# Kernel optimization log

Measured on AMD Instinct MI355X. Metric: run time of the kernel, lower is better.

## Reference

```python
import jax, jax.numpy as jnp
import numpy as np

N = 100000   # nodes
DEG = 4      # fixed out-degree (>2 so every node survives the c>2 mask)
E = N * DEG  # edges
IN = 128
H = 256


def _lin_params(key, fan_out, fan_in, bias=True):
    k1, k2 = jax.random.split(key)
    W = 0.05 * jax.random.normal(k1, (fan_out, fan_in), jnp.float32)
    if bias:
        b = 0.05 * jax.random.normal(k2, (fan_out,), jnp.float32)
        return W, b
    return W


def setup_inputs() -> dict:
    key = jax.random.key(0)
    ks = jax.random.split(key, 12)
    x = jax.random.normal(ks[0], (N, IN), jnp.float32)
    # every node has exactly DEG outgoing edges -> out-degree 4 > 2 for all nodes
    src = jnp.repeat(jnp.arange(N, dtype=jnp.int32), DEG)
    dst = jax.random.randint(ks[1], (E,), 0, N, dtype=jnp.int32)
    edge_index = jnp.stack([src, dst])  # [2, E]
    batch = jnp.zeros((N,), jnp.int32)
    Wr0, br0 = _lin_params(ks[2], H, IN)
    Ws0 = _lin_params(ks[3], H, IN, bias=False)
    Wr1, br1 = _lin_params(ks[4], H, H)
    Ws1 = _lin_params(ks[5], H, H, bias=False)
    Wr2, br2 = _lin_params(ks[6], H, H)
    Ws2 = _lin_params(ks[7], H, H, bias=False)
    Wsp1, bsp1 = _lin_params(ks[8], 1, H)
    Wsp2, bsp2 = _lin_params(ks[9], 1, H)
    Wl, bl = _lin_params(ks[10], 1, 2)
    return dict(x=x, edge_index=edge_index, batch=batch,
                Wr0=Wr0, br0=br0, Ws0=Ws0,
                Wr1=Wr1, br1=br1, Ws1=Ws1,
                Wr2=Wr2, br2=br2, Ws2=Ws2,
                Wsp1=Wsp1, bsp1=bsp1, Wsp2=Wsp2, bsp2=bsp2,
                Wl=Wl, bl=bl)


def reference(x, edge_index, batch, Wr0, br0, Ws0, Wr1, br1, Ws1,
              Wr2, br2, Ws2, Wsp1, bsp1, Wsp2, bsp2, Wl, bl):
    src, dst = edge_index[0], edge_index[1]

    def gconv(h, Wr, br, Ws):
        # PyG GraphConv(aggr='add'): out_i = W_rel @ sum_{j->i} h_j + b + W_root @ h_i
        agg = jax.ops.segment_sum(h[src], dst, num_segments=N)
        return jax.nn.relu(agg @ Wr.T + br + h @ Ws.T)

    h = gconv(x, Wr0, br0, Ws0)
    h = gconv(h, Wr1, br1, Ws1)
    h = gconv(h, Wr2, br2, Ws2)

    # unique(edge_index[0], counts) ; keep source nodes with out-degree > 2
    deg = jax.ops.segment_sum(jnp.ones((E,), h.dtype), src, num_segments=N)
    sel = jnp.nonzero(deg > 2, size=N, fill_value=0)[0]  # all N nodes by construction
    xs = h[sel].reshape(-1, 2 * H)  # pair consecutive nodes
    x1, x2 = xs[:, :H], xs[:, H:]
    out = jnp.concatenate([jax.nn.relu(x1 @ Wsp1.T + bsp1),
                           jax.nn.relu(x2 @ Wsp2.T + bsp2)], axis=1)
    y = jax.nn.sigmoid(out @ Wl.T + bl)  # split=True branch
    return y, xs, x1, x2
```

## Files before the change

kernel.cpp:

```cpp
#include <hip/hip_runtime.h>
#include <hip/hip_bf16.h>
#include <math.h>

#define NNODES 100000
#define NEDGES 400000
#define INDIM  128
#define HDIM   256
#define MAXDEG 32

#define BM 64
#define BN 256
#define MTILES 1563

typedef __attribute__((ext_vector_type(8))) short short8;
typedef __attribute__((ext_vector_type(8))) unsigned short ushort8v;
typedef __attribute__((ext_vector_type(4))) float f32x4;

__device__ __forceinline__ float bf2f(unsigned short u) {
    union { unsigned int i; float f; } v; v.i = ((unsigned int)u) << 16; return v.f;
}
__device__ __forceinline__ unsigned short f2bf(float f) {
    union { float f; unsigned int i; } v; v.f = f;
    unsigned int r = v.i + 0x7fffu + ((v.i >> 16) & 1u);
    return (unsigned short)(r >> 16);
}

__device__ __forceinline__ void async_load16(const void* g, void* l) {
    __builtin_amdgcn_global_load_lds(
        (const __attribute__((address_space(1))) unsigned int*)g,
        (__attribute__((address_space(3))) unsigned int*)l,
        16, 0, 0);
}

__device__ __forceinline__ int4 shfl4(const int4 v, int src) {
    int4 r;
    r.x = __shfl(v.x, src); r.y = __shfl(v.y, src);
    r.z = __shfl(v.z, src); r.w = __shfl(v.w, src);
    return r;
}

#define XB_BLOCKS 12500
#define W0_BLOCKS 256
#define W1_BLOCKS 512
#define EL_BLOCKS 1563
#define PREP_BLOCKS (XB_BLOCKS + W0_BLOCKS + 2 * W1_BLOCKS + EL_BLOCKS)

__global__ void prep_kernel(const float* __restrict__ x, unsigned short* __restrict__ xb,
                            const float* __restrict__ Wr0, const float* __restrict__ Ws0,
                            unsigned short* __restrict__ B0,
                            const float* __restrict__ Wr1, const float* __restrict__ Ws1,
                            unsigned short* __restrict__ B1,
                            const float* __restrict__ Wr2, const float* __restrict__ Ws2,
                            unsigned short* __restrict__ B2,
                            const int* __restrict__ ei, int* __restrict__ cnt,
                            int* __restrict__ elist) {
    int b = blockIdx.x;
    if (b < XB_BLOCKS) {
        int i = b * 256 + threadIdx.x;
        float4 v = ((const float4*)x)[i];
        ushort4 o; o.x = f2bf(v.x); o.y = f2bf(v.y); o.z = f2bf(v.z); o.w = f2bf(v.w);
        ((ushort4*)xb)[i] = o;
        return;
    }
    b -= XB_BLOCKS;
    if (b < W0_BLOCKS + 2 * W1_BLOCKS) {
        const float *Wr, *Ws; unsigned short* B; int K;
        if (b < W0_BLOCKS)               { Wr = Wr0; Ws = Ws0; B = B0; K = INDIM; }
        else if (b < W0_BLOCKS + W1_BLOCKS) { Wr = Wr1; Ws = Ws1; B = B1; K = HDIM; b -= W0_BLOCKS; }
        else                              { Wr = Wr2; Ws = Ws2; B = B2; K = HDIM; b -= W0_BLOCKS + W1_BLOCKS; }
        int idx = b * 256 + threadIdx.x;
        int n = idx / (2 * K);
        int k = idx - n * 2 * K;
        float v = (k < K) ? Wr[n * K + k] : Ws[n * K + (k - K)];
        B[idx] = f2bf(v);
        return;
    }
    b -= W0_BLOCKS + 2 * W1_BLOCKS;
    int e = b * 256 + threadIdx.x;
    if (e < NEDGES) {
        int d = ei[NEDGES + e];
        int s = ei[e];
        int pos = atomicAdd(&cnt[d], 1);
        if (pos < MAXDEG) elist[d * MAXDEG + pos] = s;
    }
}

template<int MODE, int K>
__global__ __launch_bounds__(512, 4)
void fused_gconv(const unsigned short* __restrict__ h,
                 const int* __restrict__ cnt, const int* __restrict__ elist,
                 const unsigned short* __restrict__ B, const float* __restrict__ bias,
                 unsigned short* __restrict__ hout,
                 float* __restrict__ xs, float* __restrict__ x1o, float* __restrict__ x2o,
                 const float* __restrict__ Wsp1, const float* __restrict__ Wsp2,
                 float* __restrict__ spart) {
    __shared__ __align__(16) unsigned char smem[64 * K * 2 * 2];
    unsigned short* Agg  = (unsigned short*)smem;
    unsigned short* A2sh = (unsigned short*)(smem + 64 * K * 2);

    const int tid  = threadIdx.x;
    const int lane = tid & 63;
    const int wv   = tid >> 6;
    const int m0   = blockIdx.x * BM;
    constexpr int Ktot = 2 * K;
    constexpr int SEGS = K / 8;

    const int lane31 = lane & 31;
    const int hw     = lane >> 5;
    int pn = m0 + wv * 8 + (lane >> 3);
    if (pn >= NNODES) pn = NNODES - 1;
    const int4 elv = ((const int4*)(elist + (size_t)pn * MAXDEG))[lane & 7];
    int cnode = m0 + wv * 8 + (lane & 7);
    if (cnode >= NNODES) cnode = NNODES - 1;
    const int cv = cnt[cnode];

    #pragma unroll
    for (int it = 0; it < (64 * SEGS) / 512; it++) {
        int idx = it * 512 + tid;
        int row = idx / SEGS, seg = idx % SEGS;
        int gseg = (seg & ~7) | ((seg ^ (row & 7)) & 7);
        int grow = m0 + row; if (grow >= NNODES) grow = NNODES - 1;
        async_load16(h + (size_t)grow * K + gseg * 8, &A2sh[idx * 8]);
    }

    #pragma unroll
    for (int rd = 0; rd < 4; rd++) {
        const int iw = rd * 2 + hw;
        int cA = __shfl(cv, rd * 2);
        int cB = __shfl(cv, rd * 2 + 1);
        if (cA > MAXDEG) cA = MAXDEG;
        if (cB > MAXDEG) cB = MAXDEG;
        const int c    = hw ? cB : cA;
        const int cmax = cA > cB ? cA : cB;
        const int4 e0 = shfl4(elv, iw * 8 + 0);
        const int4 e1 = shfl4(elv, iw * 8 + 1);

        if constexpr (K == 256) {
            float a[8];
            #pragma unroll
            for (int i = 0; i < 8; i++) a[i] = 0.f;
            ushort8v z = {0,0,0,0,0,0,0,0};
            ushort8v v0 = z, v1 = z, v2 = z, v3 = z;
            ushort8v w0 = z, w1 = z, w2 = z, w3 = z;
            if (c > 0) v0 = ((const ushort8v*)(h + (size_t)e0.x * 256))[lane31];
            if (c > 1) v1 = ((const ushort8v*)(h + (size_t)e0.y * 256))[lane31];
            if (c > 2) v2 = ((const ushort8v*)(h + (size_t)e0.z * 256))[lane31];
            if (c > 3) v3 = ((const ushort8v*)(h + (size_t)e0.w * 256))[lane31];
            if (cmax > 4) {
                int r2 = c - 4;
                if (r2 > 0) w0 = ((const ushort8v*)(h + (size_t)e1.x * 256))[lane31];
                if (r2 > 1) w1 = ((const ushort8v*)(h + (size_t)e1.y * 256))[lane31];
                if (r2 > 2) w2 = ((const ushort8v*)(h + (size_t)e1.z * 256))[lane31];
                if (r2 > 3) w3 = ((const ushort8v*)(h + (size_t)e1.w * 256))[lane31];
            }
            #pragma unroll
            for (int i = 0; i < 8; i++)
                a[i] += (bf2f(v0[i]) + bf2f(v1[i]) + bf2f(v2[i]) + bf2f(v3[i]))
                      + (bf2f(w0[i]) + bf2f(w1[i]) + bf2f(w2[i]) + bf2f(w3[i]));
            for (int j0 = 8; j0 < cmax; j0 += 4) {
                int4 e = shfl4(elv, iw * 8 + (j0 >> 2));
                int rem = c - j0;
                ushort8v t0 = z, t1 = z, t2 = z, t3 = z;
                if (rem > 0) t0 = ((const ushort8v*)(h + (size_t)e.x * 256))[lane31];
                if (rem > 1) t1 = ((const ushort8v*)(h + (size_t)e.y * 256))[lane31];
                if (rem > 2) t2 = ((const ushort8v*)(h + (size_t)e.z * 256))[lane31];
                if (rem > 3) t3 = ((const ushort8v*)(h + (size_t)e.w * 256))[lane31];
                #pragma unroll
                for (int i = 0; i < 8; i++)
                    a[i] += bf2f(t0[i]) + bf2f(t1[i]) + bf2f(t2[i]) + bf2f(t3[i]);
            }
            int r = wv * 8 + iw;
            int sgp = (lane31 & ~7) | ((lane31 ^ r) & 7);
            ushort8v o;
            #pragma unroll
            for (int i = 0; i < 8; i++) o[i] = f2bf(a[i]);
            *(ushort8v*)&Agg[r * 256 + sgp * 8] = o;
        } else {
            float a0 = 0.f, a1 = 0.f, a2 = 0.f, a3 = 0.f;
            ushort4 z = {0,0,0,0};
            ushort4 v0 = z, v1 = z, v2 = z, v3 = z;
            ushort4 w0 = z, w1 = z, w2 = z, w3 = z;
            if (c > 0) v0 = ((const ushort4*)(h + (size_t)e0.x * 128))[lane31];
            if (c > 1) v1 = ((const ushort4*)(h + (size_t)e0.y * 128))[lane31];
            if (c > 2) v2 = ((const ushort4*)(h + (size_t)e0.z * 128))[lane31];
            if (c > 3) v3 = ((const ushort4*)(h + (size_t)e0.w * 128))[lane31];
            if (cmax > 4) {
                int r2 = c - 4;
                if (r2 > 0) w0 = ((const ushort4*)(h + (size_t)e1.x * 128))[lane31];
                if (r2 > 1) w1 = ((const ushort4*)(h + (size_t)e1.y * 128))[lane31];
                if (r2 > 2) w2 = ((const ushort4*)(h + (size_t)e1.z * 128))[lane31];
                if (r2 > 3) w3 = ((const ushort4*)(h + (size_t)e1.w * 128))[lane31];
            }
            a0 += bf2f(v0.x) + bf2f(v1.x) + bf2f(v2.x) + bf2f(v3.x)
                + bf2f(w0.x) + bf2f(w1.x) + bf2f(w2.x) + bf2f(w3.x);
            a1 += bf2f(v0.y) + bf2f(v1.y) + bf2f(v2.y) + bf2f(v3.y)
                + bf2f(w0.y) + bf2f(w1.y) + bf2f(w2.y) + bf2f(w3.y);
            a2 += bf2f(v0.z) + bf2f(v1.z) + bf2f(v2.z) + bf2f(v3.z)
                + bf2f(w0.z) + bf2f(w1.z) + bf2f(w2.z) + bf2f(w3.z);
            a3 += bf2f(v0.w) + bf2f(v1.w) + bf2f(v2.w) + bf2f(v3.w)
                + bf2f(w0.w) + bf2f(w1.w) + bf2f(w2.w) + bf2f(w3.w);
            for (int j0 = 8; j0 < cmax; j0 += 4) {
                int4 e = shfl4(elv, iw * 8 + (j0 >> 2));
                int rem = c - j0;
                ushort4 t0 = z, t1 = z, t2 = z, t3 = z;
                if (rem > 0) t0 = ((const ushort4*)(h + (size_t)e.x * 128))[lane31];
                if (rem > 1) t1 = ((const ushort4*)(h + (size_t)e.y * 128))[lane31];
                if (rem > 2) t2 = ((const ushort4*)(h + (size_t)e.z * 128))[lane31];
                if (rem > 3) t3 = ((const ushort4*)(h + (size_t)e.w * 128))[lane31];
                a0 += bf2f(t0.x) + bf2f(t1.x) + bf2f(t2.x) + bf2f(t3.x);
                a1 += bf2f(t0.y) + bf2f(t1.y) + bf2f(t2.y) + bf2f(t3.y);
                a2 += bf2f(t0.z) + bf2f(t1.z) + bf2f(t2.z) + bf2f(t3.z);
                a3 += bf2f(t0.w) + bf2f(t1.w) + bf2f(t2.w) + bf2f(t3.w);
            }
            int r = wv * 8 + iw;
            int sg = lane31 >> 1;
            int sgp = (sg & ~7) | ((sg ^ r) & 7);
            ushort4 o; o.x = f2bf(a0); o.y = f2bf(a1); o.z = f2bf(a2); o.w = f2bf(a3);
            *(ushort4*)&Agg[r * 128 + sgp * 8 + (lane31 & 1) * 4] = o;
        }
    }

    __syncthreads();

    f32x4 acc[4][2];
    #pragma unroll
    for (int i = 0; i < 4; i++)
        #pragma unroll
        for (int j = 0; j < 2; j++)
            acc[i][j] = (f32x4){0.f, 0.f, 0.f, 0.f};

    const int l15  = lane & 15;
    const int seg0 = lane >> 4;

    #pragma unroll
    for (int k0 = 0; k0 < K; k0 += 64) {
        #pragma unroll
        for (int half = 0; half < 2; half++) {
            const int sg = (k0 >> 3) + half * 4 + seg0;
            short8 afr[4], afs[4], bwr[2], bws[2];
            #pragma unroll
            for (int nt = 0; nt < 2; nt++) {
                int nl = wv * 32 + nt * 16 + l15;
                bwr[nt] = *(const short8*)(B + (size_t)nl * Ktot + sg * 8);
                bws[nt] = *(const short8*)(B + (size_t)nl * Ktot + K + sg * 8);
            }
            #pragma unroll
            for (int mt = 0; mt < 4; mt++) {
                int ml  = mt * 16 + l15;
                int sgp = (sg & ~7) | ((sg ^ ml) & 7);
                afr[mt] = *(const short8*)&Agg [ml * K + sgp * 8];
                afs[mt] = *(const short8*)&A2sh[ml * K + sgp * 8];
            }
            #pragma unroll
            for (int mt = 0; mt < 4; mt++)
                #pragma unroll
                for (int nt = 0; nt < 2; nt++)
                    acc[mt][nt] = __builtin_amdgcn_mfma_f32_16x16x32_bf16(
                        afr[mt], bwr[nt], acc[mt][nt], 0, 0, 0);
            #pragma unroll
            for (int mt = 0; mt < 4; mt++)
                #pragma unroll
                for (int nt = 0; nt < 2; nt++)
                    acc[mt][nt] = __builtin_amdgcn_mfma_f32_16x16x32_bf16(
                        afs[mt], bws[nt], acc[mt][nt], 0, 0, 0);
        }
    }

    float* bounce = (float*)smem;
    float* wb = bounce + wv * (16 * 40);
    const int q    = lane & 3;
    const int rrow = lane >> 2;

    #pragma unroll
    for (int mt = 0; mt < 4; mt++) {
        __syncthreads();
        #pragma unroll
        for (int nt = 0; nt < 2; nt++)
            #pragma unroll
            for (int rr = 0; rr < 4; rr++)
                wb[((lane >> 4) * 4 + rr) * 40 + nt * 16 + l15] = acc[mt][nt][rr];
        __syncthreads();

        int grow = m0 + mt * 16 + rrow;
        int gc0  = wv * 32 + q * 4;
        int gc1  = gc0 + 16;
        float4 v0 = *(const float4*)(wb + rrow * 40 + q * 4);
        float4 v1 = *(const float4*)(wb + rrow * 40 + 16 + q * 4);

        if (grow < NNODES) {
            float4 b0 = *(const float4*)(bias + gc0);
            float4 b1 = *(const float4*)(bias + gc1);
            v0.x = fmaxf(v0.x + b0.x, 0.f); v0.y = fmaxf(v0.y + b0.y, 0.f);
            v0.z = fmaxf(v0.z + b0.z, 0.f); v0.w = fmaxf(v0.w + b0.w, 0.f);
            v1.x = fmaxf(v1.x + b1.x, 0.f); v1.y = fmaxf(v1.y + b1.y, 0.f);
            v1.z = fmaxf(v1.z + b1.z, 0.f); v1.w = fmaxf(v1.w + b1.w, 0.f);
            if (MODE == 0) {
                ushort4 o0, o1;
                o0.x = f2bf(v0.x); o0.y = f2bf(v0.y); o0.z = f2bf(v0.z); o0.w = f2bf(v0.w);
                o1.x = f2bf(v1.x); o1.y = f2bf(v1.y); o1.z = f2bf(v1.z); o1.w = f2bf(v1.w);
                *(ushort4*)(hout + (size_t)grow * HDIM + gc0) = o0;
                *(ushort4*)(hout + (size_t)grow * HDIM + gc1) = o1;
            } else {
                *(float4*)(xs + (size_t)grow * HDIM + gc0) = v0;
                *(float4*)(xs + (size_t)grow * HDIM + gc1) = v1;
                float* xo = (grow & 1) ? x2o : x1o;
                *(float4*)(xo + (size_t)(grow >> 1) * HDIM + gc0) = v0;
                *(float4*)(xo + (size_t)(grow >> 1) * HDIM + gc1) = v1;
                const float* wsp = (grow & 1) ? Wsp2 : Wsp1;
                float4 w0 = *(const float4*)(wsp + gc0);
                float4 w1 = *(const float4*)(wsp + gc1);
                float p = v0.x * w0.x + v0.y * w0.y + v0.z * w0.z + v0.w * w0.w
                        + v1.x * w1.x + v1.y * w1.y + v1.z * w1.z + v1.w * w1.w;
                p += __shfl_xor(p, 1);
                p += __shfl_xor(p, 2);
                if (q == 0) atomicAdd(&spart[grow], p);
            }
        }
    }
}

__global__ void finalize_kernel(const float* __restrict__ spart, const float* __restrict__ bsp1,
                                const float* __restrict__ bsp2, const float* __restrict__ Wl,
                                const float* __restrict__ bl, float* __restrict__ y) {
    int p = blockIdx.x * 256 + threadIdx.x;
    if (p < NNODES / 2) {
        float s1 = spart[2 * p]     + bsp1[0]; s1 = s1 > 0.f ? s1 : 0.f;
        float s2 = spart[2 * p + 1] + bsp2[0]; s2 = s2 > 0.f ? s2 : 0.f;
        float t = s1 * Wl[0] + s2 * Wl[1] + bl[0];
        y[p] = 1.f / (1.f + expf(-t));
    }
}

extern "C" void kernel_launch(void* const* d_in, const int* in_sizes, int n_in,
                              void* d_out, int out_size, void* d_ws, size_t ws_size,
                              hipStream_t stream) {
    const float* x    = (const float*)d_in[0];
    const int*   ei   = (const int*)d_in[1];
    const float* Wr0  = (const float*)d_in[3];
    const float* br0  = (const float*)d_in[4];
    const float* Ws0  = (const float*)d_in[5];
    const float* Wr1  = (const float*)d_in[6];
    const float* br1  = (const float*)d_in[7];
    const float* Ws1  = (const float*)d_in[8];
    const float* Wr2  = (const float*)d_in[9];
    const float* br2  = (const float*)d_in[10];
    const float* Ws2  = (const float*)d_in[11];
    const float* Wsp1 = (const float*)d_in[12];
    const float* bsp1 = (const float*)d_in[13];
    const float* Wsp2 = (const float*)d_in[14];
    const float* bsp2 = (const float*)d_in[15];
    const float* Wl   = (const float*)d_in[16];
    const float* bl   = (const float*)d_in[17];

    char* ws = (char*)d_ws;
    size_t off = 0;
    auto alloc = [&](size_t bytes) -> void* {
        void* p = ws + off;
        off += (bytes + 255) & ~(size_t)255;
        return p;
    };
    int*            cnt   = (int*)alloc((size_t)NNODES * 4);
    float*          spart = (float*)alloc((size_t)NNODES * 4);
    size_t zero_bytes = off;
    int*            elist = (int*)alloc((size_t)NNODES * MAXDEG * 4);
    unsigned short* xb    = (unsigned short*)alloc((size_t)NNODES * INDIM * 2);
    unsigned short* hA    = (unsigned short*)alloc((size_t)NNODES * HDIM * 2);
    unsigned short* hB    = (unsigned short*)alloc((size_t)NNODES * HDIM * 2);
    unsigned short* B0    = (unsigned short*)alloc((size_t)HDIM * 2 * INDIM * 2);
    unsigned short* B1    = (unsigned short*)alloc((size_t)HDIM * 2 * HDIM * 2);
    unsigned short* B2    = (unsigned short*)alloc((size_t)HDIM * 2 * HDIM * 2);

    float* y  = (float*)d_out;
    float* xs = y + 50000;
    float* x1 = xs + (size_t)50000 * 512;
    float* x2 = x1 + (size_t)50000 * 256;

    hipMemsetAsync(ws, 0, zero_bytes, stream);
    prep_kernel<<<PREP_BLOCKS, 256, 0, stream>>>(x, xb, Wr0, Ws0, B0, Wr1, Ws1, B1,
                                                 Wr2, Ws2, B2, ei, cnt, elist);

    fused_gconv<0, 128><<<MTILES, 512, 0, stream>>>(xb, cnt, elist, B0, br0, hA,
                                                    nullptr, nullptr, nullptr,
                                                    nullptr, nullptr, nullptr);
    fused_gconv<0, 256><<<MTILES, 512, 0, stream>>>(hA, cnt, elist, B1, br1, hB,
                                                    nullptr, nullptr, nullptr,
                                                    nullptr, nullptr, nullptr);
    fused_gconv<1, 256><<<MTILES, 512, 0, stream>>>(hB, cnt, elist, B2, br2, nullptr,
                                                    xs, x1, x2, Wsp1, Wsp2, spart);
    finalize_kernel<<<(NNODES / 2 + 255) / 256, 256, 0, stream>>>(
        spart, bsp1, bsp2, Wl, bl, y);
}
```

Before: 554.6 us.

## Halve row tile to 32 nodes with 4 waves each covering 64 output columns

Shrinks the row tile of the fused GraphConv kernel from 64 to 32 nodes and the block from 512 to 256 threads, doubling the grid. Each wave now computes a 32x64 output slab (2 row tiles by 4 column tiles) rather than 64x32, and the epilogue is rewritten to write wider vectors per thread. The aim is less LDS per block and more resident blocks for latency hiding during the gather phase. In exchange, every block reloads the full weight matrix for half as many rows, doubling weight traffic per node.

```diff
diff --git a/kernel.cpp b/kernel.cpp
--- a/kernel.cpp
+++ b/kernel.cpp
@@ -8,9 +8,9 @@
 #define HDIM   256
 #define MAXDEG 32
 
-#define BM 64
+#define BM 32
 #define BN 256
-#define MTILES 1563
+#define MTILES 3125
 
 typedef __attribute__((ext_vector_type(8))) short short8;
 typedef __attribute__((ext_vector_type(8))) unsigned short ushort8v;
@@ -86,7 +86,7 @@
 }
 
 template<int MODE, int K>
-__global__ __launch_bounds__(512, 4)
+__global__ __launch_bounds__(256, 5)
 void fused_gconv(const unsigned short* __restrict__ h,
                  const int* __restrict__ cnt, const int* __restrict__ elist,
                  const unsigned short* __restrict__ B, const float* __restrict__ bias,
@@ -94,9 +94,11 @@
                  float* __restrict__ xs, float* __restrict__ x1o, float* __restrict__ x2o,
                  const float* __restrict__ Wsp1, const float* __restrict__ Wsp2,
                  float* __restrict__ spart) {
-    __shared__ __align__(16) unsigned char smem[64 * K * 2 * 2];
+    constexpr int TILE_BYTES = 2 * BM * K * 2;
+    constexpr int SMEM_BYTES = TILE_BYTES > 17408 ? TILE_BYTES : 17408;
+    __shared__ __align__(16) unsigned char smem[SMEM_BYTES];
     unsigned short* Agg  = (unsigned short*)smem;
-    unsigned short* A2sh = (unsigned short*)(smem + 64 * K * 2);
+    unsigned short* A2sh = (unsigned short*)(smem + BM * K * 2);
 
     const int tid  = threadIdx.x;
     const int lane = tid & 63;
@@ -115,8 +117,8 @@
     const int cv = cnt[cnode];
 
     #pragma unroll
-    for (int it = 0; it < (64 * SEGS) / 512; it++) {
-        int idx = it * 512 + tid;
+    for (int it = 0; it < (BM * SEGS) / 256; it++) {
+        int idx = it * 256 + tid;
         int row = idx / SEGS, seg = idx % SEGS;
         int gseg = (seg & ~7) | ((seg ^ (row & 7)) & 7);
         int grow = m0 + row; if (grow >= NNODES) grow = NNODES - 1;
@@ -222,11 +224,11 @@
 
     __syncthreads();
 
-    f32x4 acc[4][2];
+    f32x4 acc[2][4];
     #pragma unroll
-    for (int i = 0; i < 4; i++)
+    for (int i = 0; i < 2; i++)
         #pragma unroll
-        for (int j = 0; j < 2; j++)
+        for (int j = 0; j < 4; j++)
             acc[i][j] = (f32x4){0.f, 0.f, 0.f, 0.f};
 
     const int l15  = lane & 15;
@@ -237,80 +239,91 @@
         #pragma unroll
         for (int half = 0; half < 2; half++) {
             const int sg = (k0 >> 3) + half * 4 + seg0;
-            short8 afr[4], afs[4], bwr[2], bws[2];
-            #pragma unroll
-            for (int nt = 0; nt < 2; nt++) {
-                int nl = wv * 32 + nt * 16 + l15;
+            short8 afr[2], afs[2], bwr[4], bws[4];
+            #pragma unroll
+            for (int nt = 0; nt < 4; nt++) {
+                int nl = wv * 64 + nt * 16 + l15;
                 bwr[nt] = *(const short8*)(B + (size_t)nl * Ktot + sg * 8);
                 bws[nt] = *(const short8*)(B + (size_t)nl * Ktot + K + sg * 8);
             }
             #pragma unroll
-            for (int mt = 0; mt < 4; mt++) {
+            for (int mt = 0; mt < 2; mt++) {
                 int ml  = mt * 16 + l15;
                 int sgp = (sg & ~7) | ((sg ^ ml) & 7);
                 afr[mt] = *(const short8*)&Agg [ml * K + sgp * 8];
                 afs[mt] = *(const short8*)&A2sh[ml * K + sgp * 8];
             }
             #pragma unroll
-            for (int mt = 0; mt < 4; mt++)
-                #pragma unroll
-                for (int nt = 0; nt < 2; nt++)
+            for (int mt = 0; mt < 2; mt++)
+                #pragma unroll
+                for (int nt = 0; nt < 4; nt++)
                     acc[mt][nt] = __builtin_amdgcn_mfma_f32_16x16x32_bf16(
                         afr[mt], bwr[nt], acc[mt][nt], 0, 0, 0);
             #pragma unroll
-            for (int mt = 0; mt < 4; mt++)
-                #pragma unroll
-                for (int nt = 0; nt < 2; nt++)
+            for (int mt = 0; mt < 2; mt++)
+                #pragma unroll
+                for (int nt = 0; nt < 4; nt++)
                     acc[mt][nt] = __builtin_amdgcn_mfma_f32_16x16x32_bf16(
                         afs[mt], bws[nt], acc[mt][nt], 0, 0, 0);
         }
     }
 
     float* bounce = (float*)smem;
-    float* wb = bounce + wv * (16 * 40);
+    float* wb = bounce + wv * (16 * 68);
     const int q    = lane & 3;
     const int rrow = lane >> 2;
 
     #pragma unroll
-    for (int mt = 0; mt < 4; mt++) {
+    for (int mt = 0; mt < 2; mt++) {
         __syncthreads();
         #pragma unroll
-        for (int nt = 0; nt < 2; nt++)
+        for (int nt = 0; nt < 4; nt++)
             #pragma unroll
             for (int rr = 0; rr < 4; rr++)
-                wb[((lane >> 4) * 4 + rr) * 40 + nt * 16 + l15] = acc[mt][nt][rr];
+                wb[((lane >> 4) * 4 + rr) * 68 + nt * 16 + l15] = acc[mt][nt][rr];
         __syncthreads();
 
         int grow = m0 + mt * 16 + rrow;
-        int gc0  = wv * 32 + q * 4;
-        int gc1  = gc0 + 16;
-        float4 v0 = *(const float4*)(wb + rrow * 40 + q * 4);
-        float4 v1 = *(const float4*)(wb + rrow * 40 + 16 + q * 4);
+        int gc   = wv * 64 + q * 16;
+        float4 v[4];
+        #pragma unroll
+        for (int s = 0; s < 4; s++)
+            v[s] = ((const float4*)(wb + rrow * 68 + q * 16))[s];
 
         if (grow < NNODES) {
-            float4 b0 = *(const float4*)(bias + gc0);
-            float4 b1 = *(const float4*)(bias + gc1);
-            v0.x = fmaxf(v0.x + b0.x, 0.f); v0.y = fmaxf(v0.y + b0.y, 0.f);
-            v0.z = fmaxf(v0.z + b0.z, 0.f); v0.w = fmaxf(v0.w + b0.w, 0.f);
-            v1.x = fmaxf(v1.x + b1.x, 0.f); v1.y = fmaxf(v1.y + b1.y, 0.f);
-            v1.z = fmaxf(v1.z + b1.z, 0.f); v1.w = fmaxf(v1.w + b1.w, 0.f);
+            const float4* bv = (const float4*)(bias + gc);
+            #pragma unroll
+            for (int s = 0; s < 4; s++) {
+                float4 b4 = bv[s];
+                v[s].x = fmaxf(v[s].x + b4.x, 0.f);
+                v[s].y = fmaxf(v[s].y + b4.y, 0.f);
+                v[s].z = fmaxf(v[s].z + b4.z, 0.f);
+                v[s].w = fmaxf(v[s].w + b4.w, 0.f);
+            }
             if (MODE == 0) {
-                ushort4 o0, o1;
-                o0.x = f2bf(v0.x); o0.y = f2bf(v0.y); o0.z = f2bf(v0.z); o0.w = f2bf(v0.w);
-                o1.x = f2bf(v1.x); o1.y = f2bf(v1.y); o1.z = f2bf(v1.z); o1.w = f2bf(v1.w);
-                *(ushort4*)(hout + (size_t)grow * HDIM + gc0) = o0;
-                *(ushort4*)(hout + (size_t)grow * HDIM + gc1) = o1;
+                ushort8v o0, o1;
+                o0[0]=f2bf(v[0].x); o0[1]=f2bf(v[0].y); o0[2]=f2bf(v[0].z); o0[3]=f2bf(v[0].w);
+                o0[4]=f2bf(v[1].x); o0[5]=f2bf(v[1].y); o0[6]=f2bf(v[1].z); o0[7]=f2bf(v[1].w);
+                o1[0]=f2bf(v[2].x); o1[1]=f2bf(v[2].y); o1[2]=f2bf(v[2].z); o1[3]=f2bf(v[2].w);
+                o1[4]=f2bf(v[3].x); o1[5]=f2bf(v[3].y); o1[6]=f2bf(v[3].z); o1[7]=f2bf(v[3].w);
+                ushort8v* dst = (ushort8v*)(hout + (size_t)grow * HDIM + gc);
+                dst[0] = o0; dst[1] = o1;
             } else {
-                *(float4*)(xs + (size_t)grow * HDIM + gc0) = v0;
-                *(float4*)(xs + (size_t)grow * HDIM + gc1) = v1;
+                float4* xsp = (float4*)(xs + (size_t)grow * HDIM + gc);
+                #pragma unroll
+                for (int s = 0; s < 4; s++) xsp[s] = v[s];
                 float* xo = (grow & 1) ? x2o : x1o;
-                *(float4*)(xo + (size_t)(grow >> 1) * HDIM + gc0) = v0;
-                *(float4*)(xo + (size_t)(grow >> 1) * HDIM + gc1) = v1;
+                float4* xop = (float4*)(xo + (size_t)(grow >> 1) * HDIM + gc);
+                #pragma unroll
+                for (int s = 0; s < 4; s++) xop[s] = v[s];
                 const float* wsp = (grow & 1) ? Wsp2 : Wsp1;
-                float4 w0 = *(const float4*)(wsp + gc0);
-                float4 w1 = *(const float4*)(wsp + gc1);
-                float p = v0.x * w0.x + v0.y * w0.y + v0.z * w0.z + v0.w * w0.w
-                        + v1.x * w1.x + v1.y * w1.y + v1.z * w1.z + v1.w * w1.w;
+                const float4* wv4 = (const float4*)(wsp + gc);
+                float p = 0.f;
+                #pragma unroll
+                for (int s = 0; s < 4; s++) {
+                    float4 w4 = wv4[s];
+                    p += v[s].x * w4.x + v[s].y * w4.y + v[s].z * w4.z + v[s].w * w4.w;
+                }
                 p += __shfl_xor(p, 1);
                 p += __shfl_xor(p, 2);
                 if (q == 0) atomicAdd(&spart[grow], p);
@@ -379,13 +392,13 @@
     prep_kernel<<<PREP_BLOCKS, 256, 0, stream>>>(x, xb, Wr0, Ws0, B0, Wr1, Ws1, B1,
                                                  Wr2, Ws2, B2, ei, cnt, elist);
 
-    fused_gconv<0, 128><<<MTILES, 512, 0, stream>>>(xb, cnt, elist, B0, br0, hA,
+    fused_gconv<0, 128><<<MTILES, 256, 0, stream>>>(xb, cnt, elist, B0, br0, hA,
                                                     nullptr, nullptr, nullptr,
                                                     nullptr, nullptr, nullptr);
-    fused_gconv<0, 256><<<MTILES, 512, 0, stream>>>(hA, cnt, elist, B1, br1, hB,
+    fused_gconv<0, 256><<<MTILES, 256, 0, stream>>>(hA, cnt, elist, B1, br1, hB,
                                                     nullptr, nullptr, nullptr,
                                                     nullptr, nullptr, nullptr);
-    fused_gconv<1, 256><<<MTILES, 512, 0, stream>>>(hB, cnt, elist, B2, br2, nullptr,
+    fused_gconv<1, 256><<<MTILES, 256, 0, stream>>>(hB, cnt, elist, B2, br2, nullptr,
                                                     xs, x1, x2, Wsp1, Wsp2, spart);
     finalize_kernel<<<(NNODES / 2 + 255) / 256, 256, 0, stream>>>(
         spart, bsp1, bsp2, Wl, bl, y);
```

Result: slower. 645.0 us (+16.3%).
